# Performance work log

Hardware: AMD Instinct MI355X
Metric: run time of the kernel (lower is better)

The kernel has to match this reference:

```python
import jax, jax.numpy as jnp
import numpy as np

B, Q, C, V = 512, 100, 81, 117  # batch, queries, obj classes (80+no-object), verbs
THRES, ALPHA, BETA = 0.7, 1.0, 0.5


def setup_inputs() -> dict:
    key = jax.random.key(0)
    k1, k2, k3, k4, k5, k6 = jax.random.split(key, 6)
    out_obj_logits = jax.random.normal(k1, (B, Q, C), jnp.float32)
    out_verb_logits = jax.random.normal(k2, (B, Q, V), jnp.float32)
    out_sub_boxes = jax.random.uniform(k3, (B, Q, 4), jnp.float32)
    out_obj_boxes = jax.random.uniform(k4, (B, Q, 4), jnp.float32)
    # correct_mat: binary verb-object compatibility [V, C-1] + ones column for no-object slot -> [V, C]
    cm = (jax.random.uniform(k5, (V, C - 1)) < 0.3).astype(jnp.float32)
    correct_mat = jnp.concatenate([cm, jnp.ones((V, 1), jnp.float32)], axis=1)
    target_sizes = jax.random.randint(k6, (B, 2), 480, 1334).astype(jnp.int64)
    return {
        'out_obj_logits': out_obj_logits,
        'out_verb_logits': out_verb_logits,
        'out_sub_boxes': out_sub_boxes,
        'out_obj_boxes': out_obj_boxes,
        'correct_mat': correct_mat,
        'target_sizes': target_sizes,
    }


def _box_cxcywh_to_xyxy(b):
    cx, cy, w, h = b[..., 0], b[..., 1], b[..., 2], b[..., 3]
    return jnp.stack([cx - 0.5 * w, cy - 0.5 * h, cx + 0.5 * w, cy + 0.5 * h], axis=-1)


def _pairwise_iou(boxes):  # boxes [Q,4] xyxy (pixel coords, +1 convention as in source)
    x1, y1, x2, y2 = boxes[:, 0], boxes[:, 1], boxes[:, 2], boxes[:, 3]
    area = (x2 - x1 + 1.0) * (y2 - y1 + 1.0)
    xx1 = jnp.maximum(x1[:, None], x1[None, :])
    yy1 = jnp.maximum(y1[:, None], y1[None, :])
    xx2 = jnp.minimum(x2[:, None], x2[None, :])
    yy2 = jnp.minimum(y2[:, None], y2[None, :])
    w = jnp.maximum(0.0, xx2 - xx1 + 1.0)
    h = jnp.maximum(0.0, yy2 - yy1 + 1.0)
    inter = w * h
    union = area[:, None] + area[None, :] - inter
    return inter / union


def _nms_one_image(sub_b, obj_b, obj_lab, max_scores):
    # Greedy pairwise triplet NMS. Grouping key in the source degenerates to the
    # object label alone (subject cat is constant, verb-label string identical),
    # so suppression applies only between detections with the same object label.
    order = jnp.argsort(-max_scores)
    sb, ob, lab = sub_b[order], obj_b[order], obj_lab[order]
    ovr = jnp.power(_pairwise_iou(sb), ALPHA) * jnp.power(_pairwise_iou(ob), BETA)
    upper = jnp.triu(jnp.ones((Q, Q), bool), 1)
    sup_mat = upper & (lab[:, None] == lab[None, :]) & (ovr > THRES)

    def body(i, supp):
        return supp | (sup_mat[i] & jnp.logical_not(supp[i]))

    supp = jax.lax.fori_loop(0, Q, body, jnp.zeros((Q,), bool))
    keep = jnp.zeros((Q,), bool).at[order].set(jnp.logical_not(supp))
    return keep  # in original query order


def reference(out_obj_logits, out_verb_logits, out_sub_boxes, out_obj_boxes, correct_mat, target_sizes):
    obj_prob = jax.nn.softmax(out_obj_logits, axis=-1)
    obj_scores = obj_prob[..., :-1].max(axis=-1)            # [B,Q]
    obj_labels = obj_prob[..., :-1].argmax(axis=-1)         # [B,Q]
    verb_scores = jax.nn.sigmoid(out_verb_logits)           # [B,Q,V]

    ts = target_sizes.astype(jnp.float32)
    img_h, img_w = ts[:, 0], ts[:, 1]
    scale_fct = jnp.stack([img_w, img_h, img_w, img_h], axis=1)  # [B,4]
    sub_boxes = _box_cxcywh_to_xyxy(out_sub_boxes) * scale_fct[:, None, :]
    obj_boxes = _box_cxcywh_to_xyxy(out_obj_boxes) * scale_fct[:, None, :]

    # masks[b,q,v] = correct_mat[v, obj_labels[b,q]]
    masks = correct_mat.T[obj_labels]                        # [B,Q,V]
    hoi_scores = verb_scores * obj_scores[..., None] * masks

    max_scores = hoi_scores.max(axis=-1)                     # [B,Q]
    keep = jax.vmap(_nms_one_image)(sub_boxes, obj_boxes, obj_labels, max_scores)
    return hoi_scores, obj_labels, sub_boxes, obj_boxes, keep
```

## Files before the change

### kernel.cpp

```cpp
#include <hip/hip_runtime.h>
#include <math.h>

#define Bn 512
#define Qn 100
#define Cn 81
#define Vn 117
#define NQ (Bn * Qn)

#define OFF_HOI  0
#define OFF_LAB  (NQ * Vn)
#define OFF_SUB  (OFF_LAB + NQ)
#define OFF_OBJ  (OFF_SUB + NQ * 4)
#define OFF_KEEP (OFF_OBJ + NQ * 4)

#define WS_SRT_OFF  65536
#define WS_ROW_OFF  (65536 + Bn * 300 * 16)

__device__ __forceinline__ float frcp(float x) { return __builtin_amdgcn_rcpf(x); }

__global__ __launch_bounds__(128) void cm_transpose(const float* __restrict__ cm,
                                                    float* __restrict__ cmT) {
    int c = blockIdx.x;
    int v = threadIdx.x;
    if (v < Vn) cmT[c * Vn + v] = cm[v * Cn + c];
}

__global__ __launch_bounds__(256) void hoi_k1(
    const float* __restrict__ obj_logits,
    const float* __restrict__ verb_logits,
    const float* __restrict__ sub_boxes,
    const float* __restrict__ obj_boxes,
    const float* __restrict__ cmT,
    const int*   __restrict__ target_sizes,
    float* __restrict__ out)
{
    __shared__ float L[16 * Cn];
    __shared__ float W[16 * Vn];

    const int tid  = threadIdx.x;
    const int base = blockIdx.x * 16;
    const int t    = tid & 15;
    const int g    = tid >> 4;
    const int idx  = base + g;
    const int b    = idx / Qn;

    {
        const float4* lgs = (const float4*)(obj_logits + (size_t)base * Cn);
        float4* Lv = (float4*)L;
        for (int i = tid; i < (16 * Cn) / 4; i += 256) Lv[i] = lgs[i];
        const float4* vls = (const float4*)(verb_logits + (size_t)base * Vn);
        float4* Wv = (float4*)W;
        for (int i = tid; i < (16 * Vn) / 4; i += 256) Wv[i] = vls[i];
    }
    __syncthreads();

    const float* lg = L + g * Cn;
    float l0 = lg[t], l1 = lg[t + 16], l2 = lg[t + 32], l3 = lg[t + 48], l4 = lg[t + 64];
    float l5 = lg[80];

    float v = l0; int vid = t;
    if (l1 > v) { v = l1; vid = t + 16; }
    if (l2 > v) { v = l2; vid = t + 32; }
    if (l3 > v) { v = l3; vid = t + 48; }
    if (l4 > v) { v = l4; vid = t + 64; }
    #pragma unroll
    for (int o = 8; o; o >>= 1) {
        float ov = __shfl_xor(v, o, 64);
        int   oi = __shfl_xor(vid, o, 64);
        if (ov > v || (ov == v && oi < vid)) { v = ov; vid = oi; }
    }

    float e = __expf(l0) + __expf(l1) + __expf(l2) + __expf(l3) + __expf(l4);
    #pragma unroll
    for (int o = 8; o; o >>= 1) e += __shfl_xor(e, o, 64);
    e += __expf(l5);

    const int   label     = vid;
    const float obj_score = __expf(v) * frcp(e);

    float* vrow = W + g * Vn;
    const float* crow = cmT + (size_t)label * Vn;

    float mx = 0.f;
    #pragma unroll
    for (int c = 0; c < 8; c++) {
        int col = t + 16 * c;
        if (col < Vn) {
            float x = vrow[col];
            float h = frcp(1.f + __expf(-x)) * obj_score * crow[col];
            vrow[col] = h;
            mx = fmaxf(mx, h);
        }
    }
    #pragma unroll
    for (int o = 8; o; o >>= 1) mx = fmaxf(mx, __shfl_xor(mx, o, 64));

    if (t == 0) {
        out[OFF_LAB + idx]  = (float)label;
        out[OFF_KEEP + idx] = mx;
    }

    if (t < 2) {
        float ih = (float)target_sizes[2 * b + 0];
        float iw = (float)target_sizes[2 * b + 1];
        const float4 bx = ((const float4*)(t == 0 ? sub_boxes : obj_boxes))[idx];
        float4 r;
        r.x = (bx.x - 0.5f * bx.z) * iw;
        r.y = (bx.y - 0.5f * bx.w) * ih;
        r.z = (bx.x + 0.5f * bx.z) * iw;
        r.w = (bx.y + 0.5f * bx.w) * ih;
        ((float4*)(out + (t == 0 ? OFF_SUB : OFF_OBJ)))[idx] = r;
    }
    __syncthreads();

    {
        const float4* Wv = (const float4*)W;
        float4* ho = (float4*)(out + OFF_HOI + (size_t)base * Vn);
        for (int i = tid; i < (16 * Vn) / 4; i += 256) ho[i] = Wv[i];
    }
}

__global__ __launch_bounds__(128) void nms_sort(const float* __restrict__ out,
                                                float4* __restrict__ srt)
{
    __shared__ float sc[Qn];
    const int b = blockIdx.x;
    const int t = threadIdx.x;

    float  kv = 0.f, labf = 0.f;
    float4 sb = make_float4(0.f,0.f,0.f,0.f), ob = sb;
    if (t < Qn) {
        kv   = out[OFF_KEEP + b * Qn + t];
        sb   = ((const float4*)(out + OFF_SUB))[b * Qn + t];
        ob   = ((const float4*)(out + OFF_OBJ))[b * Qn + t];
        labf = out[OFF_LAB + b * Qn + t];
        sc[t] = kv;
    }
    __syncthreads();

    if (t < Qn) {
        int r = 0;
        #pragma unroll 4
        for (int j = 0; j < Qn; j++) {
            float sj = sc[j];
            r += (sj > kv) || (sj == kv && j < t);
        }
        float4* S = srt + (size_t)b * 300;
        S[r]           = sb;
        S[100 + r]     = ob;
        S[200 + r]     = make_float4(
            (sb.z - sb.x + 1.f) * (sb.w - sb.y + 1.f),
            (ob.z - ob.x + 1.f) * (ob.w - ob.y + 1.f),
            labf, (float)t);
    }
}

__global__ __launch_bounds__(128) void nms_mat(const float4* __restrict__ srt,
                                               unsigned long long* __restrict__ roww)
{
    const int g = blockIdx.x >> 9;
    const int b = blockIdx.x & 511;
    const int t = threadIdx.x;
    const int sub  = t >> 6;
    const int lane = t & 63;
    const bool jv  = (t < Qn);

    const float4* S = srt + (size_t)b * 300;
    float4 js = make_float4(0.f,0.f,0.f,0.f), jo = js, jm = js;
    if (jv) { js = S[t]; jo = S[100 + t]; jm = S[200 + t]; }

    const int i0 = g * 13;
    const int i1 = (i0 + 13 < Qn - 1) ? i0 + 13 : Qn - 1;
    unsigned long long* rw = roww + ((size_t)b * Qn) * 2;

    for (int i = i0; i < i1; i++) {
        float4 is = S[i], io = S[100 + i], im = S[200 + i];
        float ww = fmaxf(0.f, fminf(is.z, js.z) - fmaxf(is.x, js.x) + 1.f);
        float hh = fmaxf(0.f, fminf(is.w, js.w) - fmaxf(is.y, js.y) + 1.f);
        float inter = ww * hh;
        float iou_s = inter / (im.x + jm.x - inter);
        ww = fmaxf(0.f, fminf(io.z, jo.z) - fmaxf(io.x, jo.x) + 1.f);
        hh = fmaxf(0.f, fminf(io.w, jo.w) - fmaxf(io.y, jo.y) + 1.f);
        inter = ww * hh;
        float iou_o = inter / (im.y + jm.y - inter);
        bool cond = jv && (t > i) && (jm.z == im.z) && (iou_s * sqrtf(iou_o) > 0.7f);
        unsigned long long m = __ballot(cond);
        if (lane == 0) rw[2 * i + sub] = m;
    }
}

__global__ __launch_bounds__(64) void nms_chain(const float4* __restrict__ srt,
                                                const ulonglong2* __restrict__ roww2,
                                                float* __restrict__ out)
{
    __shared__ ulonglong2 R[Qn];
    __shared__ int oi[Qn];
    const int b = blockIdx.x;
    const int l = threadIdx.x;

    const ulonglong2* rw = roww2 + (size_t)b * Qn;
    const float4*     M  = srt + (size_t)b * 300 + 200;

    R[l] = rw[l];
    oi[l] = (int)M[l].w;
    if (l < 36) { R[64 + l] = rw[64 + l]; oi[64 + l] = (int)M[64 + l].w; }
    __syncthreads();

    unsigned long long s0 = 0ull, s1 = 0ull;
    for (int k = 0; k < Qn - 1; k++) {
        unsigned long long dead = ((k < 64 ? s0 : s1) >> (k & 63)) & 1ull;
        if (!dead) { ulonglong2 r = R[k]; s0 |= r.x; s1 |= r.y; }
    }

    float* keepp = out + OFF_KEEP + (size_t)b * Qn;
    keepp[oi[l]] = ((s0 >> l) & 1ull) ? 0.f : 1.f;
    if (l < 36) keepp[oi[64 + l]] = ((s1 >> l) & 1ull) ? 0.f : 1.f;
}

extern "C" void kernel_launch(void* const* d_in, const int* in_sizes, int n_in,
                              void* d_out, int out_size, void* d_ws, size_t ws_size,
                              hipStream_t stream) {
    const float* obj_logits   = (const float*)d_in[0];
    const float* verb_logits  = (const float*)d_in[1];
    const float* sub_boxes    = (const float*)d_in[2];
    const float* obj_boxes    = (const float*)d_in[3];
    const float* correct_mat  = (const float*)d_in[4];
    const int*   target_sizes = (const int*)d_in[5];
    float* out = (float*)d_out;

    float*              cmT  = (float*)d_ws;
    float4*             srt  = (float4*)((char*)d_ws + WS_SRT_OFF);
    unsigned long long* roww = (unsigned long long*)((char*)d_ws + WS_ROW_OFF);

    cm_transpose<<<Cn, 128, 0, stream>>>(correct_mat, cmT);
    hoi_k1<<<NQ / 16, 256, 0, stream>>>(obj_logits, verb_logits, sub_boxes,
                                        obj_boxes, cmT, target_sizes, out);
    nms_sort<<<Bn, 128, 0, stream>>>(out, srt);
    nms_mat<<<8 * Bn, 128, 0, stream>>>(srt, roww);
    nms_chain<<<Bn, 64, 0, stream>>>(srt, (const ulonglong2*)roww, out);
}
```

Baseline: 131.9 us.

## Fuse scoring, sort, IoU matrix and NMS chain into one per-image kernel

Replaces the five-kernel pipeline with a single kernel that processes one image per block. It keeps correct_mat, the transformed boxes, scores, the sorted arrays and the suppression bitmasks in shared memory instead of workspace memory. This removes extra launches and the global round-trips between stages. In exchange it uses fewer, heavier blocks with large LDS footprints and processes queries in serial 16-row chunks, which lowers occupancy and memory-level parallelism.

```diff
diff --git a/kernel.cpp b/kernel.cpp
--- a/kernel.cpp
+++ b/kernel.cpp
@@ -13,208 +13,193 @@
 #define OFF_OBJ  (OFF_SUB + NQ * 4)
 #define OFF_KEEP (OFF_OBJ + NQ * 4)
 
-#define WS_SRT_OFF  65536
-#define WS_ROW_OFF  (65536 + Bn * 300 * 16)
-
 __device__ __forceinline__ float frcp(float x) { return __builtin_amdgcn_rcpf(x); }
 
-__global__ __launch_bounds__(128) void cm_transpose(const float* __restrict__ cm,
-                                                    float* __restrict__ cmT) {
-    int c = blockIdx.x;
-    int v = threadIdx.x;
-    if (v < Vn) cmT[c * Vn + v] = cm[v * Cn + c];
-}
-
-__global__ __launch_bounds__(256) void hoi_k1(
+__global__ __launch_bounds__(256) void hoi_fused(
     const float* __restrict__ obj_logits,
     const float* __restrict__ verb_logits,
     const float* __restrict__ sub_boxes,
     const float* __restrict__ obj_boxes,
-    const float* __restrict__ cmT,
+    const float* __restrict__ cm,
     const int*   __restrict__ target_sizes,
     float* __restrict__ out)
 {
+    __shared__ float CM[Vn * Cn];
     __shared__ float L[16 * Cn];
     __shared__ float W[16 * Vn];
-
-    const int tid  = threadIdx.x;
-    const int base = blockIdx.x * 16;
-    const int t    = tid & 15;
-    const int g    = tid >> 4;
-    const int idx  = base + g;
-    const int b    = idx / Qn;
+    __shared__ float sc[Qn];
+    __shared__ int   labs[Qn];
+    __shared__ float4 Bsub[Qn], Bobj[Qn];
+    __shared__ float4 Ssub[Qn], Sobj[Qn], Smeta[Qn];
+    __shared__ unsigned long long RR[2 * Qn];
+
+    const int tid = threadIdx.x;
+    const int b   = blockIdx.x;
+    const int t   = tid & 15;
+    const int g   = tid >> 4;
 
     {
-        const float4* lgs = (const float4*)(obj_logits + (size_t)base * Cn);
-        float4* Lv = (float4*)L;
-        for (int i = tid; i < (16 * Cn) / 4; i += 256) Lv[i] = lgs[i];
-        const float4* vls = (const float4*)(verb_logits + (size_t)base * Vn);
-        float4* Wv = (float4*)W;
-        for (int i = tid; i < (16 * Vn) / 4; i += 256) Wv[i] = vls[i];
-    }
-    __syncthreads();
-
-    const float* lg = L + g * Cn;
-    float l0 = lg[t], l1 = lg[t + 16], l2 = lg[t + 32], l3 = lg[t + 48], l4 = lg[t + 64];
-    float l5 = lg[80];
-
-    float v = l0; int vid = t;
-    if (l1 > v) { v = l1; vid = t + 16; }
-    if (l2 > v) { v = l2; vid = t + 32; }
-    if (l3 > v) { v = l3; vid = t + 48; }
-    if (l4 > v) { v = l4; vid = t + 64; }
-    #pragma unroll
-    for (int o = 8; o; o >>= 1) {
-        float ov = __shfl_xor(v, o, 64);
-        int   oi = __shfl_xor(vid, o, 64);
-        if (ov > v || (ov == v && oi < vid)) { v = ov; vid = oi; }
-    }
-
-    float e = __expf(l0) + __expf(l1) + __expf(l2) + __expf(l3) + __expf(l4);
-    #pragma unroll
-    for (int o = 8; o; o >>= 1) e += __shfl_xor(e, o, 64);
-    e += __expf(l5);
-
-    const int   label     = vid;
-    const float obj_score = __expf(v) * frcp(e);
-
-    float* vrow = W + g * Vn;
-    const float* crow = cmT + (size_t)label * Vn;
-
-    float mx = 0.f;
-    #pragma unroll
-    for (int c = 0; c < 8; c++) {
-        int col = t + 16 * c;
-        if (col < Vn) {
-            float x = vrow[col];
-            float h = frcp(1.f + __expf(-x)) * obj_score * crow[col];
-            vrow[col] = h;
-            mx = fmaxf(mx, h);
-        }
-    }
-    #pragma unroll
-    for (int o = 8; o; o >>= 1) mx = fmaxf(mx, __shfl_xor(mx, o, 64));
-
-    if (t == 0) {
-        out[OFF_LAB + idx]  = (float)label;
-        out[OFF_KEEP + idx] = mx;
-    }
-
-    if (t < 2) {
-        float ih = (float)target_sizes[2 * b + 0];
-        float iw = (float)target_sizes[2 * b + 1];
-        const float4 bx = ((const float4*)(t == 0 ? sub_boxes : obj_boxes))[idx];
+        const float4* c4 = (const float4*)cm;
+        float4* C4 = (float4*)CM;
+        for (int i = tid; i < (Vn * Cn) / 4; i += 256) C4[i] = c4[i];
+        if (tid == 0) CM[Vn * Cn - 1] = cm[Vn * Cn - 1];
+    }
+
+    const float ih = (float)target_sizes[2 * b + 0];
+    const float iw = (float)target_sizes[2 * b + 1];
+
+    if (tid < Qn) {
+        const int idx = b * Qn + tid;
+        float4 bx = ((const float4*)sub_boxes)[idx];
         float4 r;
         r.x = (bx.x - 0.5f * bx.z) * iw;
         r.y = (bx.y - 0.5f * bx.w) * ih;
         r.z = (bx.x + 0.5f * bx.z) * iw;
         r.w = (bx.y + 0.5f * bx.w) * ih;
-        ((float4*)(out + (t == 0 ? OFF_SUB : OFF_OBJ)))[idx] = r;
-    }
-    __syncthreads();
-
-    {
-        const float4* Wv = (const float4*)W;
-        float4* ho = (float4*)(out + OFF_HOI + (size_t)base * Vn);
-        for (int i = tid; i < (16 * Vn) / 4; i += 256) ho[i] = Wv[i];
-    }
-}
-
-__global__ __launch_bounds__(128) void nms_sort(const float* __restrict__ out,
-                                                float4* __restrict__ srt)
-{
-    __shared__ float sc[Qn];
-    const int b = blockIdx.x;
-    const int t = threadIdx.x;
-
-    float  kv = 0.f, labf = 0.f;
-    float4 sb = make_float4(0.f,0.f,0.f,0.f), ob = sb;
-    if (t < Qn) {
-        kv   = out[OFF_KEEP + b * Qn + t];
-        sb   = ((const float4*)(out + OFF_SUB))[b * Qn + t];
-        ob   = ((const float4*)(out + OFF_OBJ))[b * Qn + t];
-        labf = out[OFF_LAB + b * Qn + t];
-        sc[t] = kv;
-    }
-    __syncthreads();
-
-    if (t < Qn) {
+        ((float4*)(out + OFF_SUB))[idx] = r;
+        Bsub[tid] = r;
+        bx = ((const float4*)obj_boxes)[idx];
+        r.x = (bx.x - 0.5f * bx.z) * iw;
+        r.y = (bx.y - 0.5f * bx.w) * ih;
+        r.z = (bx.x + 0.5f * bx.z) * iw;
+        r.w = (bx.y + 0.5f * bx.w) * ih;
+        ((float4*)(out + OFF_OBJ))[idx] = r;
+        Bobj[tid] = r;
+    }
+
+    for (int p = 0; p < 7; p++) {
+        const int q0  = p * 16;
+        const int cnt = (q0 + 16 <= Qn) ? 16 : (Qn - q0);
+
+        {
+            const float4* lgs = (const float4*)(obj_logits + ((size_t)b * Qn + q0) * Cn);
+            float4* Lv = (float4*)L;
+            const int nL = cnt * Cn / 4;
+            for (int i = tid; i < nL; i += 256) Lv[i] = lgs[i];
+            const float4* vls = (const float4*)(verb_logits + ((size_t)b * Qn + q0) * Vn);
+            float4* Wv = (float4*)W;
+            const int nW = cnt * Vn / 4;
+            for (int i = tid; i < nW; i += 256) Wv[i] = vls[i];
+        }
+        __syncthreads();
+
+        if (g < cnt) {
+            const int q   = q0 + g;
+            const int idx = b * Qn + q;
+
+            const float* lg = L + g * Cn;
+            float l0 = lg[t], l1 = lg[t + 16], l2 = lg[t + 32], l3 = lg[t + 48], l4 = lg[t + 64];
+            float l5 = lg[80];
+
+            float v = l0; int vid = t;
+            if (l1 > v) { v = l1; vid = t + 16; }
+            if (l2 > v) { v = l2; vid = t + 32; }
+            if (l3 > v) { v = l3; vid = t + 48; }
+            if (l4 > v) { v = l4; vid = t + 64; }
+            #pragma unroll
+            for (int o = 8; o; o >>= 1) {
+                float ov = __shfl_xor(v, o, 64);
+                int   oi = __shfl_xor(vid, o, 64);
+                if (ov > v || (ov == v && oi < vid)) { v = ov; vid = oi; }
+            }
+
+            float e = __expf(l0) + __expf(l1) + __expf(l2) + __expf(l3) + __expf(l4);
+            #pragma unroll
+            for (int o = 8; o; o >>= 1) e += __shfl_xor(e, o, 64);
+            e += __expf(l5);
+
+            const int   label     = vid;
+            const float obj_score = __expf(v) * frcp(e);
+
+            float* vrow = W + g * Vn;
+            float mx = 0.f;
+            #pragma unroll
+            for (int c = 0; c < 8; c++) {
+                int col = t + 16 * c;
+                if (col < Vn) {
+                    float x = vrow[col];
+                    float h = frcp(1.f + __expf(-x)) * obj_score * CM[col * Cn + label];
+                    vrow[col] = h;
+                    mx = fmaxf(mx, h);
+                }
+            }
+            #pragma unroll
+            for (int o = 8; o; o >>= 1) mx = fmaxf(mx, __shfl_xor(mx, o, 64));
+
+            if (t == 0) {
+                out[OFF_LAB + idx] = (float)label;
+                sc[q]   = mx;
+                labs[q] = label;
+            }
+        }
+        __syncthreads();
+
+        {
+            const float4* Wv = (const float4*)W;
+            float4* ho = (float4*)(out + OFF_HOI + ((size_t)b * Qn + q0) * Vn);
+            const int nW = cnt * Vn / 4;
+            for (int i = tid; i < nW; i += 256) ho[i] = Wv[i];
+        }
+        __syncthreads();
+    }
+
+    if (tid < Qn) {
+        const float kv = sc[tid];
         int r = 0;
         #pragma unroll 4
         for (int j = 0; j < Qn; j++) {
             float sj = sc[j];
-            r += (sj > kv) || (sj == kv && j < t);
-        }
-        float4* S = srt + (size_t)b * 300;
-        S[r]           = sb;
-        S[100 + r]     = ob;
-        S[200 + r]     = make_float4(
-            (sb.z - sb.x + 1.f) * (sb.w - sb.y + 1.f),
-            (ob.z - ob.x + 1.f) * (ob.w - ob.y + 1.f),
-            labf, (float)t);
-    }
-}
-
-__global__ __launch_bounds__(128) void nms_mat(const float4* __restrict__ srt,
-                                               unsigned long long* __restrict__ roww)
-{
-    const int g = blockIdx.x >> 9;
-    const int b = blockIdx.x & 511;
-    const int t = threadIdx.x;
-    const int sub  = t >> 6;
-    const int lane = t & 63;
-    const bool jv  = (t < Qn);
-
-    const float4* S = srt + (size_t)b * 300;
-    float4 js = make_float4(0.f,0.f,0.f,0.f), jo = js, jm = js;
-    if (jv) { js = S[t]; jo = S[100 + t]; jm = S[200 + t]; }
-
-    const int i0 = g * 13;
-    const int i1 = (i0 + 13 < Qn - 1) ? i0 + 13 : Qn - 1;
-    unsigned long long* rw = roww + ((size_t)b * Qn) * 2;
-
-    for (int i = i0; i < i1; i++) {
-        float4 is = S[i], io = S[100 + i], im = S[200 + i];
-        float ww = fmaxf(0.f, fminf(is.z, js.z) - fmaxf(is.x, js.x) + 1.f);
-        float hh = fmaxf(0.f, fminf(is.w, js.w) - fmaxf(is.y, js.y) + 1.f);
-        float inter = ww * hh;
-        float iou_s = inter / (im.x + jm.x - inter);
-        ww = fmaxf(0.f, fminf(io.z, jo.z) - fmaxf(io.x, jo.x) + 1.f);
-        hh = fmaxf(0.f, fminf(io.w, jo.w) - fmaxf(io.y, jo.y) + 1.f);
-        inter = ww * hh;
-        float iou_o = inter / (im.y + jm.y - inter);
-        bool cond = jv && (t > i) && (jm.z == im.z) && (iou_s * sqrtf(iou_o) > 0.7f);
-        unsigned long long m = __ballot(cond);
-        if (lane == 0) rw[2 * i + sub] = m;
-    }
-}
-
-__global__ __launch_bounds__(64) void nms_chain(const float4* __restrict__ srt,
-                                                const ulonglong2* __restrict__ roww2,
-                                                float* __restrict__ out)
-{
-    __shared__ ulonglong2 R[Qn];
-    __shared__ int oi[Qn];
-    const int b = blockIdx.x;
-    const int l = threadIdx.x;
-
-    const ulonglong2* rw = roww2 + (size_t)b * Qn;
-    const float4*     M  = srt + (size_t)b * 300 + 200;
-
-    R[l] = rw[l];
-    oi[l] = (int)M[l].w;
-    if (l < 36) { R[64 + l] = rw[64 + l]; oi[64 + l] = (int)M[64 + l].w; }
+            r += (sj > kv) || (sj == kv && j < tid);
+        }
+        float4 sb = Bsub[tid], ob = Bobj[tid];
+        Ssub[r] = sb;
+        Sobj[r] = ob;
+        Smeta[r] = make_float4((sb.z - sb.x + 1.f) * (sb.w - sb.y + 1.f),
+                               (ob.z - ob.x + 1.f) * (ob.w - ob.y + 1.f),
+                               (float)labs[tid], (float)tid);
+    }
     __syncthreads();
 
-    unsigned long long s0 = 0ull, s1 = 0ull;
-    for (int k = 0; k < Qn - 1; k++) {
-        unsigned long long dead = ((k < 64 ? s0 : s1) >> (k & 63)) & 1ull;
-        if (!dead) { ulonglong2 r = R[k]; s0 |= r.x; s1 |= r.y; }
-    }
-
-    float* keepp = out + OFF_KEEP + (size_t)b * Qn;
-    keepp[oi[l]] = ((s0 >> l) & 1ull) ? 0.f : 1.f;
-    if (l < 36) keepp[oi[64 + l]] = ((s1 >> l) & 1ull) ? 0.f : 1.f;
+    {
+        const int tc   = tid & 127;
+        const int half = tid >> 7;
+        const int lane = tid & 63;
+        const int sub  = (tid >> 6) & 1;
+        const bool jv  = (tc < Qn);
+
+        float4 js = make_float4(0.f, 0.f, 0.f, 0.f), jo = js, jm = js;
+        if (jv) { js = Ssub[tc]; jo = Sobj[tc]; jm = Smeta[tc]; }
+
+        const int i0 = half ? 50 : 0;
+        const int i1 = half ? (Qn - 1) : 50;
+        for (int i = i0; i < i1; i++) {
+            float4 is = Ssub[i], io = Sobj[i], im = Smeta[i];
+            float ww = fmaxf(0.f, fminf(is.z, js.z) - fmaxf(is.x, js.x) + 1.f);
+            float hh = fmaxf(0.f, fminf(is.w, js.w) - fmaxf(is.y, js.y) + 1.f);
+            float inter = ww * hh;
+            float iou_s = inter / (im.x + jm.x - inter);
+            ww = fmaxf(0.f, fminf(io.z, jo.z) - fmaxf(io.x, jo.x) + 1.f);
+            hh = fmaxf(0.f, fminf(io.w, jo.w) - fmaxf(io.y, jo.y) + 1.f);
+            inter = ww * hh;
+            float iou_o = inter / (im.y + jm.y - inter);
+            bool cond = jv && (tc > i) && (jm.z == im.z) && (iou_s * sqrtf(iou_o) > 0.7f);
+            unsigned long long m = __ballot(cond);
+            if (lane == 0) RR[2 * i + sub] = m;
+        }
+    }
+    __syncthreads();
+
+    if (tid < 64) {
+        unsigned long long s0 = 0ull, s1 = 0ull;
+        for (int k = 0; k < Qn - 1; k++) {
+            unsigned long long dead = ((k < 64 ? s0 : s1) >> (k & 63)) & 1ull;
+            if (!dead) { s0 |= RR[2 * k]; s1 |= RR[2 * k + 1]; }
+        }
+        float* keepp = out + OFF_KEEP + (size_t)b * Qn;
+        keepp[(int)Smeta[tid].w] = ((s0 >> tid) & 1ull) ? 0.f : 1.f;
+        if (tid < 36)
+            keepp[(int)Smeta[64 + tid].w] = ((s1 >> tid) & 1ull) ? 0.f : 1.f;
+    }
 }
 
 extern "C" void kernel_launch(void* const* d_in, const int* in_sizes, int n_in,
@@ -227,15 +212,8 @@
     const float* correct_mat  = (const float*)d_in[4];
     const int*   target_sizes = (const int*)d_in[5];
     float* out = (float*)d_out;
-
-    float*              cmT  = (float*)d_ws;
-    float4*             srt  = (float4*)((char*)d_ws + WS_SRT_OFF);
-    unsigned long long* roww = (unsigned long long*)((char*)d_ws + WS_ROW_OFF);
-
-    cm_transpose<<<Cn, 128, 0, stream>>>(correct_mat, cmT);
-    hoi_k1<<<NQ / 16, 256, 0, stream>>>(obj_logits, verb_logits, sub_boxes,
-                                        obj_boxes, cmT, target_sizes, out);
-    nms_sort<<<Bn, 128, 0, stream>>>(out, srt);
-    nms_mat<<<8 * Bn, 128, 0, stream>>>(srt, roww);
-    nms_chain<<<Bn, 64, 0, stream>>>(srt, (const ulonglong2*)roww, out);
+    (void)d_ws; (void)ws_size; (void)in_sizes; (void)n_in; (void)out_size;
+
+    hoi_fused<<<Bn, 256, 0, stream>>>(obj_logits, verb_logits, sub_boxes,
+                                      obj_boxes, correct_mat, target_sizes, out);
 }
```

Result: slower. 140.3 us (+6.4%).
